# Performance work log

Hardware: AMD Instinct MI355X
Metric: run time of the kernel (lower is better)

The kernel has to match this reference:

```python
import jax, jax.numpy as jnp
import numpy as np

N = 3_000_000  # batch of deformation gradients


def setup_inputs() -> dict:
    key = jax.random.key(0)
    eye = jnp.eye(3, dtype=jnp.float32)
    noise = jax.random.normal(key, (N, 3, 3), dtype=jnp.float32)
    # near-identity deformation gradients so det(F) > 0 (log J well-defined)
    F = eye[None, :, :] + 0.05 * noise
    return {"F": F}


def _energy(F):
    """Strain energy density W(F) per sample. F: [N,3,3]."""
    g = jnp.array([4.0, 0.5, 0.5], dtype=F.dtype)  # transversely isotropic structural tensor (diagonal)
    C = jnp.einsum('nji,njk->nik', F, F)           # right Cauchy-Green C = F^T F, [N,3,3]
    I1 = jnp.trace(C, axis1=1, axis2=2)            # tr(C)
    J = jnp.linalg.det(F)                          # det(F)
    cofC = (J ** 2)[:, None, None] * jnp.linalg.inv(C)  # cof(C) = det(C) C^{-1}, det(C) = J^2
    I4 = jnp.einsum('nii,i->n', C, g)              # tr(C G), G diagonal
    I5 = jnp.einsum('nii,i->n', cofC, g)           # tr(cof(C) G)
    return 8.0 * I1 + 10.0 * J ** 2 - 56.0 * jnp.log(J) + 0.2 * (I4 ** 2 + I5 ** 2) - 44.0


def reference(F):
    # P = dW/dF, computed per sample; grad of the batch-sum gives per-sample grads
    return jax.grad(lambda f: jnp.sum(_energy(f)))(F)
```

## Files before the change

### kernel.cpp

```cpp
#include <hip/hip_runtime.h>


typedef float f4 __attribute__((ext_vector_type(4)));

#define SAMPLES_PER_BLOCK 1024
#define F4_PER_BLOCK (SAMPLES_PER_BLOCK * 9 / 4)

__global__ __launch_bounds__(256, 4) void pk1_grad_kernel(
    const f4* __restrict__ Fin, f4* __restrict__ Pout, int total4)
{
    __shared__ f4 lds4[F4_PER_BLOCK];
    const int t = threadIdx.x;
    const int base4 = blockIdx.x * F4_PER_BLOCK;

#pragma unroll
    for (int j = 0; j < 9; ++j) {
        int i = j * 256 + t;
        int g = base4 + i;
        f4 v;
        if (g < total4) v = Fin[g];
        else { v.x = 1.0f; v.y = 0.0f; v.z = 0.0f; v.w = 1.0f; }
        lds4[i] = v;
    }
    __syncthreads();

    float buf[36];
#pragma unroll
    for (int q = 0; q < 9; ++q) {
        f4 v = lds4[t * 9 + q];
        buf[4 * q]     = v.x;
        buf[4 * q + 1] = v.y;
        buf[4 * q + 2] = v.z;
        buf[4 * q + 3] = v.w;
    }

#pragma unroll
    for (int s = 0; s < 4; ++s) {
        float f[9];
#pragma unroll
        for (int k = 0; k < 9; ++k) f[k] = buf[s * 9 + k];

        float c00 = f[4]*f[8] - f[5]*f[7];
        float c01 = f[5]*f[6] - f[3]*f[8];
        float c02 = f[3]*f[7] - f[4]*f[6];
        float c10 = f[2]*f[7] - f[1]*f[8];
        float c11 = f[0]*f[8] - f[2]*f[6];
        float c12 = f[1]*f[6] - f[0]*f[7];
        float c20 = f[1]*f[5] - f[2]*f[4];
        float c21 = f[2]*f[3] - f[0]*f[5];
        float c22 = f[0]*f[4] - f[1]*f[3];
        float J    = f[0]*c00 + f[1]*c01 + f[2]*c02;
        float invJ = 1.0f / J;

        float C00 = f[0]*f[0] + f[3]*f[3] + f[6]*f[6];
        float C11 = f[1]*f[1] + f[4]*f[4] + f[7]*f[7];
        float C22 = f[2]*f[2] + f[5]*f[5] + f[8]*f[8];
        float C01 = f[0]*f[1] + f[3]*f[4] + f[6]*f[7];
        float C02 = f[0]*f[2] + f[3]*f[5] + f[6]*f[8];
        float C12 = f[1]*f[2] + f[4]*f[5] + f[7]*f[8];

        float I4 = 4.0f*C00 + 0.5f*(C11 + C22);

        float K00 = C11*C22 - C12*C12;
        float K11 = C00*C22 - C02*C02;
        float K22 = C00*C11 - C01*C01;
        float K01 = C02*C12 - C01*C22;
        float K02 = C01*C12 - C02*C11;
        float K12 = C01*C02 - C00*C12;

        float I5 = 4.0f*K00 + 0.5f*(K11 + K22);

        float J2    = J * J;
        float alpha = (20.0f*J2 - 56.0f + 0.8f*I5*I5) * invJ;
        float beta  = 0.8f * I4;
        float gamma = -0.8f * I5 * invJ;

        float cf[3][3] = {{c00,c01,c02},{c10,c11,c12},{c20,c21,c22}};
        float K[3][3]  = {{K00,K01,K02},{K01,K11,K12},{K02,K12,K22}};
        const float gv[3] = {4.0f, 0.5f, 0.5f};

#pragma unroll
        for (int i = 0; i < 3; ++i) {
            float a0 = cf[i][0] * 4.0f;
            float a1 = cf[i][1] * 0.5f;
            float a2 = cf[i][2] * 0.5f;
#pragma unroll
            for (int j = 0; j < 3; ++j) {
                float M = a0 * K[0][j] + a1 * K[1][j] + a2 * K[2][j];
                buf[s * 9 + 3 * i + j] =
                      (16.0f + beta * gv[j]) * f[3 * i + j]
                    + alpha * cf[i][j]
                    + gamma * M;
            }
        }
    }

    __syncthreads();

#pragma unroll
    for (int q = 0; q < 9; ++q) {
        f4 v;
        v.x = buf[4 * q];
        v.y = buf[4 * q + 1];
        v.z = buf[4 * q + 2];
        v.w = buf[4 * q + 3];
        lds4[t * 9 + q] = v;
    }
    __syncthreads();

#pragma unroll
    for (int j = 0; j < 9; ++j) {
        int i = j * 256 + t;
        int g = base4 + i;
        if (g < total4) Pout[g] = lds4[i];
    }
}

extern "C" void kernel_launch(void* const* d_in, const int* in_sizes, int n_in,
                              void* d_out, int out_size, void* d_ws, size_t ws_size,
                              hipStream_t stream) {
    const f4* F = (const f4*)d_in[0];
    f4* P = (f4*)d_out;
    int total4 = in_sizes[0] / 4;
    int blocks = (total4 + F4_PER_BLOCK - 1) / F4_PER_BLOCK;
    pk1_grad_kernel<<<blocks, 256, 0, stream>>>(F, P, total4);
}
```

Measured before the change: 44.94 us.

## Make kernel persistent with register prefetch of the next tile

```diff
diff --git a/kernel.cpp b/kernel.cpp
--- a/kernel.cpp
+++ b/kernel.cpp
@@ -3,116 +3,133 @@
 
 typedef float f4 __attribute__((ext_vector_type(4)));
 
-#define SAMPLES_PER_BLOCK 1024
-#define F4_PER_BLOCK (SAMPLES_PER_BLOCK * 9 / 4)
+#define TPB 256
+#define SAMPLES_PER_TILE 1024
+#define F4_PER_TILE (SAMPLES_PER_TILE * 9 / 4)
+#define NBLOCKS 1024
 
-__global__ __launch_bounds__(256, 4) void pk1_grad_kernel(
-    const f4* __restrict__ Fin, f4* __restrict__ Pout, int total4)
+__global__ __launch_bounds__(TPB) void pk1_grad_kernel(
+    const f4* __restrict__ Fin, f4* __restrict__ Pout, int total4, int ntiles)
 {
-    __shared__ f4 lds4[F4_PER_BLOCK];
+    __shared__ f4 lds[F4_PER_TILE];
     const int t = threadIdx.x;
-    const int base4 = blockIdx.x * F4_PER_BLOCK;
 
+    f4 pre[9];
+    {
+        const int base4 = blockIdx.x * F4_PER_TILE;
 #pragma unroll
-    for (int j = 0; j < 9; ++j) {
-        int i = j * 256 + t;
-        int g = base4 + i;
-        f4 v;
-        if (g < total4) v = Fin[g];
-        else { v.x = 1.0f; v.y = 0.0f; v.z = 0.0f; v.w = 1.0f; }
-        lds4[i] = v;
-    }
-    __syncthreads();
-
-    float buf[36];
-#pragma unroll
-    for (int q = 0; q < 9; ++q) {
-        f4 v = lds4[t * 9 + q];
-        buf[4 * q]     = v.x;
-        buf[4 * q + 1] = v.y;
-        buf[4 * q + 2] = v.z;
-        buf[4 * q + 3] = v.w;
-    }
-
-#pragma unroll
-    for (int s = 0; s < 4; ++s) {
-        float f[9];
-#pragma unroll
-        for (int k = 0; k < 9; ++k) f[k] = buf[s * 9 + k];
-
-        float c00 = f[4]*f[8] - f[5]*f[7];
-        float c01 = f[5]*f[6] - f[3]*f[8];
-        float c02 = f[3]*f[7] - f[4]*f[6];
-        float c10 = f[2]*f[7] - f[1]*f[8];
-        float c11 = f[0]*f[8] - f[2]*f[6];
-        float c12 = f[1]*f[6] - f[0]*f[7];
-        float c20 = f[1]*f[5] - f[2]*f[4];
-        float c21 = f[2]*f[3] - f[0]*f[5];
-        float c22 = f[0]*f[4] - f[1]*f[3];
-        float J    = f[0]*c00 + f[1]*c01 + f[2]*c02;
-        float invJ = 1.0f / J;
-
-        float C00 = f[0]*f[0] + f[3]*f[3] + f[6]*f[6];
-        float C11 = f[1]*f[1] + f[4]*f[4] + f[7]*f[7];
-        float C22 = f[2]*f[2] + f[5]*f[5] + f[8]*f[8];
-        float C01 = f[0]*f[1] + f[3]*f[4] + f[6]*f[7];
-        float C02 = f[0]*f[2] + f[3]*f[5] + f[6]*f[8];
-        float C12 = f[1]*f[2] + f[4]*f[5] + f[7]*f[8];
-
-        float I4 = 4.0f*C00 + 0.5f*(C11 + C22);
-
-        float K00 = C11*C22 - C12*C12;
-        float K11 = C00*C22 - C02*C02;
-        float K22 = C00*C11 - C01*C01;
-        float K01 = C02*C12 - C01*C22;
-        float K02 = C01*C12 - C02*C11;
-        float K12 = C01*C02 - C00*C12;
-
-        float I5 = 4.0f*K00 + 0.5f*(K11 + K22);
-
-        float J2    = J * J;
-        float alpha = (20.0f*J2 - 56.0f + 0.8f*I5*I5) * invJ;
-        float beta  = 0.8f * I4;
-        float gamma = -0.8f * I5 * invJ;
-
-        float cf[3][3] = {{c00,c01,c02},{c10,c11,c12},{c20,c21,c22}};
-        float K[3][3]  = {{K00,K01,K02},{K01,K11,K12},{K02,K12,K22}};
-        const float gv[3] = {4.0f, 0.5f, 0.5f};
-
-#pragma unroll
-        for (int i = 0; i < 3; ++i) {
-            float a0 = cf[i][0] * 4.0f;
-            float a1 = cf[i][1] * 0.5f;
-            float a2 = cf[i][2] * 0.5f;
-#pragma unroll
-            for (int j = 0; j < 3; ++j) {
-                float M = a0 * K[0][j] + a1 * K[1][j] + a2 * K[2][j];
-                buf[s * 9 + 3 * i + j] =
-                      (16.0f + beta * gv[j]) * f[3 * i + j]
-                    + alpha * cf[i][j]
-                    + gamma * M;
-            }
+        for (int q = 0; q < 9; ++q) {
+            int g = base4 + q * TPB + t;
+            if (g < total4) pre[q] = Fin[g];
+            else { pre[q].x = 1.0f; pre[q].y = 0.0f; pre[q].z = 0.0f; pre[q].w = 1.0f; }
         }
     }
 
-    __syncthreads();
+    for (int tile = blockIdx.x; tile < ntiles; tile += NBLOCKS) {
+        const int base4 = tile * F4_PER_TILE;
 
 #pragma unroll
-    for (int q = 0; q < 9; ++q) {
-        f4 v;
-        v.x = buf[4 * q];
-        v.y = buf[4 * q + 1];
-        v.z = buf[4 * q + 2];
-        v.w = buf[4 * q + 3];
-        lds4[t * 9 + q] = v;
-    }
-    __syncthreads();
+        for (int q = 0; q < 9; ++q) lds[q * TPB + t] = pre[q];
+        __syncthreads();
+
+        const int ntile = tile + NBLOCKS;
+        if (ntile < ntiles) {
+            const int nbase4 = ntile * F4_PER_TILE;
+#pragma unroll
+            for (int q = 0; q < 9; ++q) {
+                int g = nbase4 + q * TPB + t;
+                if (g < total4) pre[q] = Fin[g];
+                else { pre[q].x = 1.0f; pre[q].y = 0.0f; pre[q].z = 0.0f; pre[q].w = 1.0f; }
+            }
+        }
+
+        float buf[36];
+#pragma unroll
+        for (int q = 0; q < 9; ++q) {
+            f4 v = lds[t * 9 + q];
+            buf[4 * q]     = v.x;
+            buf[4 * q + 1] = v.y;
+            buf[4 * q + 2] = v.z;
+            buf[4 * q + 3] = v.w;
+        }
 
 #pragma unroll
-    for (int j = 0; j < 9; ++j) {
-        int i = j * 256 + t;
-        int g = base4 + i;
-        if (g < total4) Pout[g] = lds4[i];
+        for (int s = 0; s < 4; ++s) {
+            float f[9];
+#pragma unroll
+            for (int k = 0; k < 9; ++k) f[k] = buf[s * 9 + k];
+
+            float c00 = f[4]*f[8] - f[5]*f[7];
+            float c01 = f[5]*f[6] - f[3]*f[8];
+            float c02 = f[3]*f[7] - f[4]*f[6];
+            float c10 = f[2]*f[7] - f[1]*f[8];
+            float c11 = f[0]*f[8] - f[2]*f[6];
+            float c12 = f[1]*f[6] - f[0]*f[7];
+            float c20 = f[1]*f[5] - f[2]*f[4];
+            float c21 = f[2]*f[3] - f[0]*f[5];
+            float c22 = f[0]*f[4] - f[1]*f[3];
+            float J    = f[0]*c00 + f[1]*c01 + f[2]*c02;
+            float invJ = 1.0f / J;
+
+            float C00 = f[0]*f[0] + f[3]*f[3] + f[6]*f[6];
+            float C11 = f[1]*f[1] + f[4]*f[4] + f[7]*f[7];
+            float C22 = f[2]*f[2] + f[5]*f[5] + f[8]*f[8];
+            float C01 = f[0]*f[1] + f[3]*f[4] + f[6]*f[7];
+            float C02 = f[0]*f[2] + f[3]*f[5] + f[6]*f[8];
+            float C12 = f[1]*f[2] + f[4]*f[5] + f[7]*f[8];
+
+            float I4 = 4.0f*C00 + 0.5f*(C11 + C22);
+
+            float K00 = C11*C22 - C12*C12;
+            float K11 = C00*C22 - C02*C02;
+            float K22 = C00*C11 - C01*C01;
+            float K01 = C02*C12 - C01*C22;
+            float K02 = C01*C12 - C02*C11;
+            float K12 = C01*C02 - C00*C12;
+
+            float I5 = 4.0f*K00 + 0.5f*(K11 + K22);
+
+            float J2    = J * J;
+            float alpha = (20.0f*J2 - 56.0f + 0.8f*I5*I5) * invJ;
+            float beta  = 0.8f * I4;
+            float gamma = -0.8f * I5 * invJ;
+
+            float cf[3][3] = {{c00,c01,c02},{c10,c11,c12},{c20,c21,c22}};
+            float K[3][3]  = {{K00,K01,K02},{K01,K11,K12},{K02,K12,K22}};
+            const float gv[3] = {4.0f, 0.5f, 0.5f};
+
+#pragma unroll
+            for (int i = 0; i < 3; ++i) {
+                float a0 = cf[i][0] * 4.0f;
+                float a1 = cf[i][1] * 0.5f;
+                float a2 = cf[i][2] * 0.5f;
+#pragma unroll
+                for (int j = 0; j < 3; ++j) {
+                    float M = a0 * K[0][j] + a1 * K[1][j] + a2 * K[2][j];
+                    buf[s * 9 + 3 * i + j] =
+                          (16.0f + beta * gv[j]) * f[3 * i + j]
+                        + alpha * cf[i][j]
+                        + gamma * M;
+                }
+            }
+        }
+
+#pragma unroll
+        for (int q = 0; q < 9; ++q) {
+            f4 v;
+            v.x = buf[4 * q];
+            v.y = buf[4 * q + 1];
+            v.z = buf[4 * q + 2];
+            v.w = buf[4 * q + 3];
+            lds[t * 9 + q] = v;
+        }
+        __syncthreads();
+
+#pragma unroll
+        for (int q = 0; q < 9; ++q) {
+            int g = base4 + q * TPB + t;
+            if (g < total4) Pout[g] = lds[q * TPB + t];
+        }
     }
 }
 
@@ -122,6 +139,6 @@
     const f4* F = (const f4*)d_in[0];
     f4* P = (f4*)d_out;
     int total4 = in_sizes[0] / 4;
-    int blocks = (total4 + F4_PER_BLOCK - 1) / F4_PER_BLOCK;
-    pk1_grad_kernel<<<blocks, 256, 0, stream>>>(F, P, total4);
+    int ntiles = (total4 + F4_PER_TILE - 1) / F4_PER_TILE;
+    pk1_grad_kernel<<<NBLOCKS, TPB, 0, stream>>>(F, P, total4, ntiles);
 }
```

After: 39.45 us. 12.2% less time.
